# Kernel tuning notes

Measured on AMD Instinct MI355X. Metric: run time of the kernel, lower is better.

The kernel has to match this reference:

```python
import jax, jax.numpy as jnp
import numpy as np

BS, NUM_VISIT, MAX_FEAT, MAX_TARGET = 32, 6, 12, 16
NUM_FEAT, NUM_REL, HIDDEN, REDUCED, OUT = 1992, 11, 128, 256, 90
GAMMA = 0.1


def setup_inputs() -> dict:
    key = jax.random.key(0)
    ks = jax.random.split(key, 20)
    u = lambda k, shape: jax.random.uniform(k, shape, dtype=jnp.float32)
    # one/multi-hot-like dense float inputs (per docstring)
    feat_index = (u(ks[0], (BS, NUM_VISIT, MAX_FEAT, NUM_FEAT)) < 0.01).astype(jnp.float32)
    neighbor_index = (u(ks[1], (BS, NUM_VISIT, MAX_FEAT, MAX_TARGET, NUM_FEAT)) < 0.001).astype(jnp.float32)
    rel_index = (u(ks[2], (BS, NUM_VISIT, MAX_FEAT, MAX_TARGET, NUM_REL)) < 0.2).astype(jnp.float32)
    # parameters (torch.rand init in the original; xavier for embedding)
    bound = float(np.sqrt(6.0 / (NUM_FEAT + HIDDEN)))
    emb_weight = jax.random.uniform(ks[3], (NUM_FEAT, HIDDEN), dtype=jnp.float32, minval=-bound, maxval=bound)
    return {
        "feat_index": feat_index,
        "neighbor_index": neighbor_index,
        "rel_index": rel_index,
        "emb_weight": emb_weight,
        "W_edge": u(ks[4], (NUM_REL, HIDDEN)),
        "W_v": u(ks[5], (REDUCED, HIDDEN)),
        "W_r": u(ks[6], (REDUCED, HIDDEN)),
        "b_v": u(ks[7], (REDUCED,)),
        "b_r": u(ks[8], (REDUCED,)),
        "W_alpha": u(ks[9], (NUM_FEAT,)),
        "b_alpha": u(ks[10], (MAX_FEAT,)),
        "W_beta": u(ks[11], (MAX_FEAT,)),
        "b_beta": u(ks[12], (NUM_VISIT,)),
        "W_l": u(ks[13], (REDUCED, REDUCED)),
        "b_l": u(ks[14], (REDUCED,)),
        "fc_W": u(ks[15], (OUT, 2 * REDUCED)) * 0.05,
        "fc_b": u(ks[16], (OUT,)) * 0.05,
    }


def reference(feat_index, neighbor_index, rel_index, emb_weight, W_edge, W_v, W_r,
              b_v, b_r, W_alpha, b_alpha, W_beta, b_beta, W_l, b_l, fc_W, fc_b):
    num_visit = feat_index.shape[1]
    # decay buffer lamb[i] = exp(-gamma*(num_visit - i))
    lamb = jnp.exp(-GAMMA * (num_visit - jnp.arange(num_visit, dtype=feat_index.dtype)))

    # node-level attention alpha: (b,v,m)
    alpha = jax.nn.softmax(jnp.einsum('n,bvmn->bvm', W_alpha, feat_index) + b_alpha)
    # visit-level attention beta: (b,v), modulated by temporal decay
    beta = jnp.tanh(jnp.einsum('m,bvm->bv', W_beta, alpha) + b_beta) * lamb

    # reduced node embeddings: (num_feat, reduced)
    reduced_emb = emb_weight @ W_v.T + b_v
    # attention-weighted neighbor aggregation; sum over targets t fused in
    attn = alpha * beta[:, :, None]                       # (b,v,m)
    node_agg = jnp.einsum('bvm,bvmtn,nr->bvmr', attn, neighbor_index, reduced_emb)

    # reduced edge (relation) embeddings: (num_rel, reduced)
    reduced_edge = W_edge @ W_r.T + b_r
    edge_agg = jnp.einsum('bvmtr,rd->bvmd', rel_index, reduced_edge)  # sum over t fused

    agg = node_agg + edge_agg                             # (b,v,m,reduced)
    # einsum('dd, bvfd -> bvfd') in torch takes the diagonal of W_l
    h = jax.nn.relu(jnp.diagonal(W_l) * agg + b_l)        # (b,v,m,reduced)

    h_g = h.sum(axis=(1, 2))                              # (b, reduced)
    # einsum('bvmn,bvmr->bvnr').sum(n).sum(v) == contract over v,m,n
    h_p = jnp.einsum('bvm,bvmr->br', feat_index.sum(-1), h)

    z_joint = jnp.concatenate([h_g, h_p], axis=-1)        # (b, 2*reduced)
    return jax.nn.sigmoid(z_joint @ fc_W.T + fc_b)
```

## Files before the change

kernel.cpp:

```cpp
#include <hip/hip_runtime.h>
#include <math.h>

#define BS   32
#define NV   6
#define MF   12
#define MT   16
#define NF   1992
#define NR   11
#define HID  128
#define RED  256
#define OUTD 90
#define GAMMA 0.1f
#define NZCAP 1024

typedef float f4_t __attribute__((ext_vector_type(4)));

#define WS_HG    0
#define WS_HP    (WS_HG + BS*RED)
#define WS_ATTN  (WS_HP + BS*RED)
#define WS_FSUM  (WS_ATTN + BS*NV*MF)
#define WS_REMB  (WS_FSUM + BS*NV*MF)
#define WS_REDGE (WS_REMB + NF*RED)
#define WS_WTV   (WS_REDGE + NR*RED)
#define WS_WTR   (WS_WTV + HID*RED)
#define WS_FCWT  (WS_WTR + HID*RED)
#define WS_DIAG  (WS_FCWT + 2*RED*OUTD)
#define WS_CNT   (WS_DIAG + RED)
#define WS_RSUM  (WS_CNT + BS*NV*MF)
#define WS_NZN   (WS_RSUM + BS*NV*MF*NR)
#define WS_NZV   (WS_NZN + BS*NV*MF*NZCAP)

#define STREAM_BLOCKS (BS*NV*MF)
#define N_ZERO (2*BS*RED)
#define N_WTV  (HID*RED)
#define N_WTR  (HID*RED)
#define N_FCWT (2*RED*OUTD)
#define N_DIAG RED
#define PREP_ELEMS (N_ZERO + N_WTV + N_WTR + N_FCWT + N_DIAG)
#define PREP_BLOCKS (PREP_ELEMS / 256)

__global__ __launch_bounds__(256) void k_stream_prep_attn(
        const float* __restrict__ nbr, const float* __restrict__ rel,
        const float* __restrict__ W_v, const float* __restrict__ W_r,
        const float* __restrict__ fc_W, const float* __restrict__ W_l,
        const float* __restrict__ feat, const float* __restrict__ W_alpha,
        const float* __restrict__ b_alpha, const float* __restrict__ W_beta,
        const float* __restrict__ b_beta,
        float* __restrict__ ws_base,
        float* __restrict__ WT_v, float* __restrict__ WT_r, float* __restrict__ fcWT,
        float* __restrict__ diag,
        int* __restrict__ cnt_g, float* __restrict__ rsum_g,
        int* __restrict__ nzn_g, float* __restrict__ nzv_g,
        float* __restrict__ attn_ws, float* __restrict__ fsum_ws) {
    int blk = blockIdx.x;
    int tid = threadIdx.x;

    if (blk < STREAM_BLOCKS) {
        int bvm = blk;
        __shared__ int   nz_n[NZCAP];
        __shared__ float nz_v[NZCAP];
        __shared__ int   cnt;
        if (tid == 0) cnt = 0;
        const f4_t* base = (const f4_t*)(nbr + (size_t)bvm * MT * NF);
        f4_t a0 = (f4_t)(0.f);
        f4_t a1 = (f4_t)(0.f);
        const bool has1 = (tid + 256) < (NF / 4);
        #pragma unroll 4
        for (int t = 0; t < MT; ++t) {
            const f4_t* r4 = base + t * (NF / 4);
            a0 += __builtin_nontemporal_load(r4 + tid);
            if (has1) a1 += __builtin_nontemporal_load(r4 + tid + 256);
        }
        float rs = 0.f;
        if (tid < NR) {
            const float* rb = rel + (size_t)bvm * MT * NR;
            #pragma unroll
            for (int t = 0; t < MT; ++t) rs += rb[t * NR + tid];
        }
        __syncthreads();
        int nb = tid * 4;
        #pragma unroll
        for (int c = 0; c < 4; ++c)
            if (a0[c] != 0.f) {
                int p = atomicAdd(&cnt, 1);
                if (p < NZCAP) { nz_n[p] = nb + c; nz_v[p] = a0[c]; }
            }
        if (has1) {
            nb = (tid + 256) * 4;
            #pragma unroll
            for (int c = 0; c < 4; ++c)
                if (a1[c] != 0.f) {
                    int p = atomicAdd(&cnt, 1);
                    if (p < NZCAP) { nz_n[p] = nb + c; nz_v[p] = a1[c]; }
                }
        }
        __syncthreads();
        int c = min(cnt, NZCAP);
        if (tid == 0) cnt_g[bvm] = c;
        if (tid < NR) rsum_g[bvm * NR + tid] = rs;
        for (int i = tid; i < c; i += 256) {
            nzn_g[bvm * NZCAP + i] = nz_n[i];
            nzv_g[bvm * NZCAP + i] = nz_v[i];
        }
        return;
    }
    blk -= STREAM_BLOCKS;

    if (blk < PREP_BLOCKS) {
        int i = blk * 256 + tid;
        if (i < N_ZERO) {
            ws_base[i] = 0.f;
        } else if (i < N_ZERO + N_WTV) {
            int j = i - N_ZERO;
            int k = j >> 8, r = j & 255;
            WT_v[j] = W_v[r * HID + k];
        } else if (i < N_ZERO + N_WTV + N_WTR) {
            int j = i - (N_ZERO + N_WTV);
            int k = j >> 8, r = j & 255;
            WT_r[j] = W_r[r * HID + k];
        } else if (i < N_ZERO + N_WTV + N_WTR + N_FCWT) {
            int j = i - (N_ZERO + N_WTV + N_WTR);
            int jj = j / OUTD, o = j - jj * OUTD;
            fcWT[j] = fc_W[o * (2 * RED) + jj];
        } else {
            int j = i - (N_ZERO + N_WTV + N_WTR + N_FCWT);
            diag[j] = W_l[(size_t)j * RED + j];
        }
        return;
    }

    int bv   = blk - PREP_BLOCKS;
    int v    = bv % NV;
    int wave = tid >> 6;
    int lane = tid & 63;
    __shared__ float dot12[MF], fs12[MF];
    const float* base = feat + (size_t)bv * MF * NF;
    for (int m = wave; m < MF; m += 4) {
        const float4* rw = (const float4*)(base + (size_t)m * NF);
        const float4* wa = (const float4*)W_alpha;
        float da = 0.f, fs = 0.f;
        for (int i = lane; i < NF / 4; i += 64) {
            float4 x = rw[i];
            float4 w = wa[i];
            da += w.x * x.x + w.y * x.y + w.z * x.z + w.w * x.w;
            fs += x.x + x.y + x.z + x.w;
        }
        #pragma unroll
        for (int off = 32; off > 0; off >>= 1) {
            da += __shfl_xor(da, off);
            fs += __shfl_xor(fs, off);
        }
        if (lane == 0) { dot12[m] = da; fs12[m] = fs; }
    }
    __syncthreads();
    if (tid == 0) {
        float logits[MF];
        float mx = -1e30f;
        for (int m = 0; m < MF; ++m) { logits[m] = dot12[m] + b_alpha[m]; mx = fmaxf(mx, logits[m]); }
        float s = 0.f;
        for (int m = 0; m < MF; ++m) { logits[m] = expf(logits[m] - mx); s += logits[m]; }
        float inv = 1.f / s;
        float bdot = 0.f;
        for (int m = 0; m < MF; ++m) { logits[m] *= inv; bdot += W_beta[m] * logits[m]; }
        float lamb = expf(-GAMMA * (float)(NV - v));
        float beta = tanhf(bdot + b_beta[v]) * lamb;
        for (int m = 0; m < MF; ++m) {
            attn_ws[bv * MF + m] = logits[m] * beta;
            fsum_ws[bv * MF + m] = fs12[m];
        }
    }
}

#define NPB 8
#define NODE_BLOCKS (NF / NPB)
__global__ __launch_bounds__(256) void k_reduce(
        const float* __restrict__ emb, const float* __restrict__ W_edge,
        const float* __restrict__ WT_v, const float* __restrict__ WT_r,
        const float* __restrict__ b_v, const float* __restrict__ b_r,
        float* __restrict__ remb, float* __restrict__ redge) {
    int blk = blockIdx.x;
    int tid = threadIdx.x;
    if (blk < NODE_BLOCKS) {
        __shared__ float rows[NPB][HID];
        int n0 = blk * NPB;
        for (int i = tid; i < NPB * HID; i += 256)
            rows[i >> 7][i & 127] = emb[(size_t)n0 * HID + i];
        __syncthreads();
        float bv0 = b_v[tid];
        float a0 = bv0, a1 = bv0, a2 = bv0, a3 = bv0;
        float a4 = bv0, a5 = bv0, a6 = bv0, a7 = bv0;
        #pragma unroll 4
        for (int k = 0; k < HID; ++k) {
            float w = WT_v[k * RED + tid];
            a0 += rows[0][k] * w;
            a1 += rows[1][k] * w;
            a2 += rows[2][k] * w;
            a3 += rows[3][k] * w;
            a4 += rows[4][k] * w;
            a5 += rows[5][k] * w;
            a6 += rows[6][k] * w;
            a7 += rows[7][k] * w;
        }
        float* dst = remb + (size_t)n0 * RED + tid;
        dst[0*RED] = a0; dst[1*RED] = a1; dst[2*RED] = a2; dst[3*RED] = a3;
        dst[4*RED] = a4; dst[5*RED] = a5; dst[6*RED] = a6; dst[7*RED] = a7;
    } else {
        int e = blk - NODE_BLOCKS;
        __shared__ float row[HID];
        if (tid < HID) row[tid] = W_edge[e * HID + tid];
        __syncthreads();
        float acc = b_r[tid];
        #pragma unroll 4
        for (int k = 0; k < HID; ++k)
            acc += row[k] * WT_r[k * RED + tid];
        redge[e * RED + tid] = acc;
    }
}

__global__ __launch_bounds__(256) void k_gather(
        const float* __restrict__ remb, const float* __restrict__ redge,
        const int* __restrict__ cnt_g, const float* __restrict__ rsum_g,
        const int* __restrict__ nzn_g, const float* __restrict__ nzv_g,
        const float* __restrict__ attn_ws, const float* __restrict__ fsum_ws,
        const float* __restrict__ diag, const float* __restrict__ b_l,
        float* __restrict__ h_g, float* __restrict__ h_p) {
    int bvm = blockIdx.x;
    int b   = bvm / (NV * MF);
    int tid = threadIdx.x;
    __shared__ int   nz_n[NZCAP];
    __shared__ float nz_v[NZCAP];
    __shared__ float rsum[NR];
    int c = cnt_g[bvm];
    if (tid < NR) rsum[tid] = rsum_g[bvm * NR + tid];
    for (int i = tid; i < c; i += 256) {
        nz_n[i] = nzn_g[bvm * NZCAP + i];
        nz_v[i] = nzv_g[bvm * NZCAP + i];
    }
    __syncthreads();
    int r = tid;
    float node = 0.f;
    for (int i = 0; i < c; ++i)
        node += nz_v[i] * remb[(size_t)nz_n[i] * RED + r];
    float edge = 0.f;
    #pragma unroll
    for (int j = 0; j < NR; ++j)
        edge += rsum[j] * redge[j * RED + r];
    float a  = attn_ws[bvm];
    float fs = fsum_ws[bvm];
    float agg = a * node + edge;
    float h = fmaxf(0.f, diag[r] * agg + b_l[r]);
    atomicAdd(&h_g[b * RED + r], h);
    atomicAdd(&h_p[b * RED + r], fs * h);
}

__global__ __launch_bounds__(256) void k_out(
        const float* __restrict__ h_g, const float* __restrict__ h_p,
        const float* __restrict__ fcWT, const float* __restrict__ fc_b,
        float* __restrict__ out) {
    int b   = blockIdx.x;
    int tid = threadIdx.x;
    __shared__ float z[2 * RED];
    __shared__ float part[2][OUTD];
    for (int j = tid; j < RED; j += 256) {
        z[j]       = h_g[b * RED + j];
        z[RED + j] = h_p[b * RED + j];
    }
    __syncthreads();
    int o = tid & 127, half = tid >> 7;
    if (o < OUTD) {
        float acc = 0.f;
        int j0 = half * RED;
        #pragma unroll 8
        for (int j = j0; j < j0 + RED; ++j)
            acc += z[j] * fcWT[j * OUTD + o];
        part[half][o] = acc;
    }
    __syncthreads();
    if (tid < OUTD) {
        float acc = part[0][tid] + part[1][tid] + fc_b[tid];
        out[b * OUTD + tid] = 1.f / (1.f + expf(-acc));
    }
}

extern "C" void kernel_launch(void* const* d_in, const int* in_sizes, int n_in,
                              void* d_out, int out_size, void* d_ws, size_t ws_size,
                              hipStream_t stream) {
    const float* feat    = (const float*)d_in[0];
    const float* nbr     = (const float*)d_in[1];
    const float* rel     = (const float*)d_in[2];
    const float* emb     = (const float*)d_in[3];
    const float* W_edge  = (const float*)d_in[4];
    const float* W_v     = (const float*)d_in[5];
    const float* W_r     = (const float*)d_in[6];
    const float* b_v     = (const float*)d_in[7];
    const float* b_r     = (const float*)d_in[8];
    const float* W_alpha = (const float*)d_in[9];
    const float* b_alpha = (const float*)d_in[10];
    const float* W_beta  = (const float*)d_in[11];
    const float* b_beta  = (const float*)d_in[12];
    const float* W_l     = (const float*)d_in[13];
    const float* b_l     = (const float*)d_in[14];
    const float* fc_W    = (const float*)d_in[15];
    const float* fc_b    = (const float*)d_in[16];

    float* ws    = (float*)d_ws;
    float* hg    = ws + WS_HG;
    float* hp    = ws + WS_HP;
    float* attn  = ws + WS_ATTN;
    float* fsum  = ws + WS_FSUM;
    float* remb  = ws + WS_REMB;
    float* redge = ws + WS_REDGE;
    float* WT_v  = ws + WS_WTV;
    float* WT_r  = ws + WS_WTR;
    float* fcWT  = ws + WS_FCWT;
    float* diag  = ws + WS_DIAG;
    int*   cnt_g = (int*)(ws + WS_CNT);
    float* rsum_g= ws + WS_RSUM;
    int*   nzn_g = (int*)(ws + WS_NZN);
    float* nzv_g = ws + WS_NZV;

    k_stream_prep_attn<<<STREAM_BLOCKS + PREP_BLOCKS + BS * NV, 256, 0, stream>>>(
        nbr, rel, W_v, W_r, fc_W, W_l, feat, W_alpha, b_alpha, W_beta, b_beta,
        ws, WT_v, WT_r, fcWT, diag, cnt_g, rsum_g, nzn_g, nzv_g, attn, fsum);
    k_reduce<<<NODE_BLOCKS + NR, 256, 0, stream>>>(
        emb, W_edge, WT_v, WT_r, b_v, b_r, remb, redge);
    k_gather<<<BS * NV * MF, 256, 0, stream>>>(
        remb, redge, cnt_g, rsum_g, nzn_g, nzv_g, attn, fsum, diag, b_l, hg, hp);
    k_out<<<BS, 256, 0, stream>>>(hg, hp, fcWT, fc_b, (float*)d_out);
}
```

Baseline: 450.8 us.

## Fuse neighbor streaming into gather and merge prep with embedding reduction

The neighbor-index streaming and nonzero compaction move into the gather kernel, so the nonzero lists stay in shared memory instead of going through global memory. The embedding and relation reductions are folded into the first kernel and read transposed weights through shared-memory tiles, which removes the separate transpose pass. This cuts one launch and the global write/read of the nonzero lists. The nonzero cap is halved, which assumes the compacted list per row stays small, and the gather loop gets four independent accumulators.

```diff
diff --git a/kernel.cpp b/kernel.cpp
--- a/kernel.cpp
+++ b/kernel.cpp
@@ -11,7 +11,7 @@
 #define RED  256
 #define OUTD 90
 #define GAMMA 0.1f
-#define NZCAP 1024
+#define NZCAP 512
 
 typedef float f4_t __attribute__((ext_vector_type(4)));
 
@@ -21,206 +21,145 @@
 #define WS_FSUM  (WS_ATTN + BS*NV*MF)
 #define WS_REMB  (WS_FSUM + BS*NV*MF)
 #define WS_REDGE (WS_REMB + NF*RED)
-#define WS_WTV   (WS_REDGE + NR*RED)
-#define WS_WTR   (WS_WTV + HID*RED)
-#define WS_FCWT  (WS_WTR + HID*RED)
+#define WS_FCWT  (WS_REDGE + NR*RED)
 #define WS_DIAG  (WS_FCWT + 2*RED*OUTD)
-#define WS_CNT   (WS_DIAG + RED)
-#define WS_RSUM  (WS_CNT + BS*NV*MF)
-#define WS_NZN   (WS_RSUM + BS*NV*MF*NR)
-#define WS_NZV   (WS_NZN + BS*NV*MF*NZCAP)
-
-#define STREAM_BLOCKS (BS*NV*MF)
+
 #define N_ZERO (2*BS*RED)
-#define N_WTV  (HID*RED)
-#define N_WTR  (HID*RED)
 #define N_FCWT (2*RED*OUTD)
-#define N_DIAG RED
-#define PREP_ELEMS (N_ZERO + N_WTV + N_WTR + N_FCWT + N_DIAG)
-#define PREP_BLOCKS (PREP_ELEMS / 256)
-
-__global__ __launch_bounds__(256) void k_stream_prep_attn(
-        const float* __restrict__ nbr, const float* __restrict__ rel,
-        const float* __restrict__ W_v, const float* __restrict__ W_r,
-        const float* __restrict__ fc_W, const float* __restrict__ W_l,
+#define ZERO_BLOCKS (N_ZERO/256)
+#define PREP2_BLOCKS ((N_FCWT+RED)/256)
+#define ATTN_BLOCKS (BS*NV)
+#define NPB 8
+#define REMB_BLOCKS (NF/NPB)
+#define REDGE_BLOCKS 2
+#define K1_BLOCKS (ZERO_BLOCKS+PREP2_BLOCKS+ATTN_BLOCKS+REMB_BLOCKS+REDGE_BLOCKS)
+
+__global__ __launch_bounds__(256) void k1_prep_attn_reduce(
         const float* __restrict__ feat, const float* __restrict__ W_alpha,
         const float* __restrict__ b_alpha, const float* __restrict__ W_beta,
         const float* __restrict__ b_beta,
-        float* __restrict__ ws_base,
-        float* __restrict__ WT_v, float* __restrict__ WT_r, float* __restrict__ fcWT,
+        const float* __restrict__ emb, const float* __restrict__ W_edge,
+        const float* __restrict__ W_v, const float* __restrict__ W_r,
+        const float* __restrict__ b_v, const float* __restrict__ b_r,
+        const float* __restrict__ fc_W, const float* __restrict__ W_l,
+        float* __restrict__ ws_base, float* __restrict__ fcWT,
         float* __restrict__ diag,
-        int* __restrict__ cnt_g, float* __restrict__ rsum_g,
-        int* __restrict__ nzn_g, float* __restrict__ nzv_g,
-        float* __restrict__ attn_ws, float* __restrict__ fsum_ws) {
-    int blk = blockIdx.x;
-    int tid = threadIdx.x;
-
-    if (blk < STREAM_BLOCKS) {
-        int bvm = blk;
-        __shared__ int   nz_n[NZCAP];
-        __shared__ float nz_v[NZCAP];
-        __shared__ int   cnt;
-        if (tid == 0) cnt = 0;
-        const f4_t* base = (const f4_t*)(nbr + (size_t)bvm * MT * NF);
-        f4_t a0 = (f4_t)(0.f);
-        f4_t a1 = (f4_t)(0.f);
-        const bool has1 = (tid + 256) < (NF / 4);
-        #pragma unroll 4
-        for (int t = 0; t < MT; ++t) {
-            const f4_t* r4 = base + t * (NF / 4);
-            a0 += __builtin_nontemporal_load(r4 + tid);
-            if (has1) a1 += __builtin_nontemporal_load(r4 + tid + 256);
-        }
-        float rs = 0.f;
-        if (tid < NR) {
-            const float* rb = rel + (size_t)bvm * MT * NR;
-            #pragma unroll
-            for (int t = 0; t < MT; ++t) rs += rb[t * NR + tid];
-        }
-        __syncthreads();
-        int nb = tid * 4;
-        #pragma unroll
-        for (int c = 0; c < 4; ++c)
-            if (a0[c] != 0.f) {
-                int p = atomicAdd(&cnt, 1);
-                if (p < NZCAP) { nz_n[p] = nb + c; nz_v[p] = a0[c]; }
-            }
-        if (has1) {
-            nb = (tid + 256) * 4;
-            #pragma unroll
-            for (int c = 0; c < 4; ++c)
-                if (a1[c] != 0.f) {
-                    int p = atomicAdd(&cnt, 1);
-                    if (p < NZCAP) { nz_n[p] = nb + c; nz_v[p] = a1[c]; }
-                }
-        }
-        __syncthreads();
-        int c = min(cnt, NZCAP);
-        if (tid == 0) cnt_g[bvm] = c;
-        if (tid < NR) rsum_g[bvm * NR + tid] = rs;
-        for (int i = tid; i < c; i += 256) {
-            nzn_g[bvm * NZCAP + i] = nz_n[i];
-            nzv_g[bvm * NZCAP + i] = nz_v[i];
-        }
-        return;
-    }
-    blk -= STREAM_BLOCKS;
-
-    if (blk < PREP_BLOCKS) {
-        int i = blk * 256 + tid;
-        if (i < N_ZERO) {
-            ws_base[i] = 0.f;
-        } else if (i < N_ZERO + N_WTV) {
-            int j = i - N_ZERO;
-            int k = j >> 8, r = j & 255;
-            WT_v[j] = W_v[r * HID + k];
-        } else if (i < N_ZERO + N_WTV + N_WTR) {
-            int j = i - (N_ZERO + N_WTV);
-            int k = j >> 8, r = j & 255;
-            WT_r[j] = W_r[r * HID + k];
-        } else if (i < N_ZERO + N_WTV + N_WTR + N_FCWT) {
-            int j = i - (N_ZERO + N_WTV + N_WTR);
-            int jj = j / OUTD, o = j - jj * OUTD;
-            fcWT[j] = fc_W[o * (2 * RED) + jj];
-        } else {
-            int j = i - (N_ZERO + N_WTV + N_WTR + N_FCWT);
-            diag[j] = W_l[(size_t)j * RED + j];
-        }
-        return;
-    }
-
-    int bv   = blk - PREP_BLOCKS;
-    int v    = bv % NV;
-    int wave = tid >> 6;
-    int lane = tid & 63;
-    __shared__ float dot12[MF], fs12[MF];
-    const float* base = feat + (size_t)bv * MF * NF;
-    for (int m = wave; m < MF; m += 4) {
-        const float4* rw = (const float4*)(base + (size_t)m * NF);
-        const float4* wa = (const float4*)W_alpha;
-        float da = 0.f, fs = 0.f;
-        for (int i = lane; i < NF / 4; i += 64) {
-            float4 x = rw[i];
-            float4 w = wa[i];
-            da += w.x * x.x + w.y * x.y + w.z * x.z + w.w * x.w;
-            fs += x.x + x.y + x.z + x.w;
-        }
-        #pragma unroll
-        for (int off = 32; off > 0; off >>= 1) {
-            da += __shfl_xor(da, off);
-            fs += __shfl_xor(fs, off);
-        }
-        if (lane == 0) { dot12[m] = da; fs12[m] = fs; }
-    }
-    __syncthreads();
-    if (tid == 0) {
-        float logits[MF];
-        float mx = -1e30f;
-        for (int m = 0; m < MF; ++m) { logits[m] = dot12[m] + b_alpha[m]; mx = fmaxf(mx, logits[m]); }
-        float s = 0.f;
-        for (int m = 0; m < MF; ++m) { logits[m] = expf(logits[m] - mx); s += logits[m]; }
-        float inv = 1.f / s;
-        float bdot = 0.f;
-        for (int m = 0; m < MF; ++m) { logits[m] *= inv; bdot += W_beta[m] * logits[m]; }
-        float lamb = expf(-GAMMA * (float)(NV - v));
-        float beta = tanhf(bdot + b_beta[v]) * lamb;
-        for (int m = 0; m < MF; ++m) {
-            attn_ws[bv * MF + m] = logits[m] * beta;
-            fsum_ws[bv * MF + m] = fs12[m];
-        }
-    }
-}
-
-#define NPB 8
-#define NODE_BLOCKS (NF / NPB)
-__global__ __launch_bounds__(256) void k_reduce(
-        const float* __restrict__ emb, const float* __restrict__ W_edge,
-        const float* __restrict__ WT_v, const float* __restrict__ WT_r,
-        const float* __restrict__ b_v, const float* __restrict__ b_r,
+        float* __restrict__ attn_ws, float* __restrict__ fsum_ws,
         float* __restrict__ remb, float* __restrict__ redge) {
     int blk = blockIdx.x;
     int tid = threadIdx.x;
-    if (blk < NODE_BLOCKS) {
-        __shared__ float rows[NPB][HID];
-        int n0 = blk * NPB;
-        for (int i = tid; i < NPB * HID; i += 256)
-            rows[i >> 7][i & 127] = emb[(size_t)n0 * HID + i];
+
+    __shared__ float dot12[MF], fs12[MF];
+    __shared__ float rows[NPB][HID];
+    __shared__ float wT[32][RED + 1];
+
+    if (blk < ZERO_BLOCKS) {
+        ws_base[blk * 256 + tid] = 0.f;
+        return;
+    }
+    blk -= ZERO_BLOCKS;
+
+    if (blk < PREP2_BLOCKS) {
+        int i = blk * 256 + tid;
+        if (i < N_FCWT) {
+            int jj = i / OUTD, o = i - jj * OUTD;
+            fcWT[i] = fc_W[o * (2 * RED) + jj];
+        } else {
+            int j = i - N_FCWT;
+            diag[j] = W_l[(size_t)j * RED + j];
+        }
+        return;
+    }
+    blk -= PREP2_BLOCKS;
+
+    if (blk < ATTN_BLOCKS) {
+        int bv   = blk;
+        int v    = bv % NV;
+        int wave = tid >> 6;
+        int lane = tid & 63;
+        const float* base = feat + (size_t)bv * MF * NF;
+        for (int m = wave; m < MF; m += 4) {
+            const float4* rw = (const float4*)(base + (size_t)m * NF);
+            const float4* wa = (const float4*)W_alpha;
+            float da = 0.f, fs = 0.f;
+            for (int i = lane; i < NF / 4; i += 64) {
+                float4 x = rw[i];
+                float4 w = wa[i];
+                da += w.x * x.x + w.y * x.y + w.z * x.z + w.w * x.w;
+                fs += x.x + x.y + x.z + x.w;
+            }
+            #pragma unroll
+            for (int off = 32; off > 0; off >>= 1) {
+                da += __shfl_xor(da, off);
+                fs += __shfl_xor(fs, off);
+            }
+            if (lane == 0) { dot12[m] = da; fs12[m] = fs; }
+        }
         __syncthreads();
-        float bv0 = b_v[tid];
-        float a0 = bv0, a1 = bv0, a2 = bv0, a3 = bv0;
-        float a4 = bv0, a5 = bv0, a6 = bv0, a7 = bv0;
-        #pragma unroll 4
-        for (int k = 0; k < HID; ++k) {
-            float w = WT_v[k * RED + tid];
-            a0 += rows[0][k] * w;
-            a1 += rows[1][k] * w;
-            a2 += rows[2][k] * w;
-            a3 += rows[3][k] * w;
-            a4 += rows[4][k] * w;
-            a5 += rows[5][k] * w;
-            a6 += rows[6][k] * w;
-            a7 += rows[7][k] * w;
-        }
-        float* dst = remb + (size_t)n0 * RED + tid;
-        dst[0*RED] = a0; dst[1*RED] = a1; dst[2*RED] = a2; dst[3*RED] = a3;
-        dst[4*RED] = a4; dst[5*RED] = a5; dst[6*RED] = a6; dst[7*RED] = a7;
-    } else {
-        int e = blk - NODE_BLOCKS;
-        __shared__ float row[HID];
-        if (tid < HID) row[tid] = W_edge[e * HID + tid];
+        if (tid == 0) {
+            float logits[MF];
+            float mx = -1e30f;
+            for (int m = 0; m < MF; ++m) { logits[m] = dot12[m] + b_alpha[m]; mx = fmaxf(mx, logits[m]); }
+            float s = 0.f;
+            for (int m = 0; m < MF; ++m) { logits[m] = expf(logits[m] - mx); s += logits[m]; }
+            float inv = 1.f / s;
+            float bdot = 0.f;
+            for (int m = 0; m < MF; ++m) { logits[m] *= inv; bdot += W_beta[m] * logits[m]; }
+            float lamb = expf(-GAMMA * (float)(NV - v));
+            float beta = tanhf(bdot + b_beta[v]) * lamb;
+            for (int m = 0; m < MF; ++m) {
+                attn_ws[bv * MF + m] = logits[m] * beta;
+                fsum_ws[bv * MF + m] = fs12[m];
+            }
+        }
+        return;
+    }
+    blk -= ATTN_BLOCKS;
+
+    bool isEdge = (blk >= REMB_BLOCKS);
+    const float* src  = isEdge ? W_edge : emb;
+    const float* Wm   = isEdge ? W_r : W_v;
+    const float* bias = isEdge ? b_r : b_v;
+    float* dst        = isEdge ? redge : remb;
+    int n0    = (isEdge ? (blk - REMB_BLOCKS) : blk) * NPB;
+    int rowsN = isEdge ? min(NPB, NR - n0) : NPB;
+
+    for (int idx = tid; idx < rowsN * HID; idx += 256)
+        rows[idx >> 7][idx & 127] = src[(size_t)n0 * HID + idx];
+
+    float bb = bias[tid];
+    float a0 = bb, a1 = bb, a2 = bb, a3 = bb, a4 = bb, a5 = bb, a6 = bb, a7 = bb;
+    for (int k0 = 0; k0 < HID; k0 += 32) {
+        for (int idx = tid; idx < 32 * RED; idx += 256) {
+            int rr = idx >> 5, kk = idx & 31;
+            wT[kk][rr] = Wm[rr * HID + k0 + kk];
+        }
         __syncthreads();
-        float acc = b_r[tid];
-        #pragma unroll 4
-        for (int k = 0; k < HID; ++k)
-            acc += row[k] * WT_r[k * RED + tid];
-        redge[e * RED + tid] = acc;
-    }
+        #pragma unroll
+        for (int kk = 0; kk < 32; ++kk) {
+            float w = wT[kk][tid];
+            int k = k0 + kk;
+            a0 += rows[0][k] * w; a1 += rows[1][k] * w;
+            a2 += rows[2][k] * w; a3 += rows[3][k] * w;
+            a4 += rows[4][k] * w; a5 += rows[5][k] * w;
+            a6 += rows[6][k] * w; a7 += rows[7][k] * w;
+        }
+        __syncthreads();
+    }
+    float* d0 = dst + (size_t)n0 * RED + tid;
+    if (0 < rowsN) d0[0 * RED] = a0;
+    if (1 < rowsN) d0[1 * RED] = a1;
+    if (2 < rowsN) d0[2 * RED] = a2;
+    if (3 < rowsN) d0[3 * RED] = a3;
+    if (4 < rowsN) d0[4 * RED] = a4;
+    if (5 < rowsN) d0[5 * RED] = a5;
+    if (6 < rowsN) d0[6 * RED] = a6;
+    if (7 < rowsN) d0[7 * RED] = a7;
 }
 
-__global__ __launch_bounds__(256) void k_gather(
+__global__ __launch_bounds__(256) void k2_stream_gather(
+        const float* __restrict__ nbr, const float* __restrict__ rel,
         const float* __restrict__ remb, const float* __restrict__ redge,
-        const int* __restrict__ cnt_g, const float* __restrict__ rsum_g,
-        const int* __restrict__ nzn_g, const float* __restrict__ nzv_g,
         const float* __restrict__ attn_ws, const float* __restrict__ fsum_ws,
         const float* __restrict__ diag, const float* __restrict__ b_l,
         float* __restrict__ h_g, float* __restrict__ h_p) {
@@ -229,28 +168,75 @@
     int tid = threadIdx.x;
     __shared__ int   nz_n[NZCAP];
     __shared__ float nz_v[NZCAP];
-    __shared__ float rsum[NR];
-    int c = cnt_g[bvm];
-    if (tid < NR) rsum[tid] = rsum_g[bvm * NR + tid];
-    for (int i = tid; i < c; i += 256) {
-        nz_n[i] = nzn_g[bvm * NZCAP + i];
-        nz_v[i] = nzv_g[bvm * NZCAP + i];
+    __shared__ float rsum_s[NR];
+    __shared__ int   cnt;
+    __shared__ float s_attn, s_fsum;
+    if (tid == 0) { cnt = 0; s_attn = attn_ws[bvm]; s_fsum = fsum_ws[bvm]; }
+
+    int r = tid;
+    float dg = diag[r];
+    float bl = b_l[r];
+    float rg[NR];
+    #pragma unroll
+    for (int j = 0; j < NR; ++j) rg[j] = redge[j * RED + r];
+
+    const f4_t* base = (const f4_t*)(nbr + (size_t)bvm * MT * NF);
+    f4_t a0 = (f4_t)(0.f);
+    f4_t a1 = (f4_t)(0.f);
+    const bool has1 = (tid + 256) < (NF / 4);
+    #pragma unroll 4
+    for (int t = 0; t < MT; ++t) {
+        const f4_t* r4 = base + t * (NF / 4);
+        a0 += __builtin_nontemporal_load(r4 + tid);
+        if (has1) a1 += __builtin_nontemporal_load(r4 + tid + 256);
+    }
+    float rs = 0.f;
+    if (tid < NR) {
+        const float* rb = rel + (size_t)bvm * MT * NR;
+        #pragma unroll
+        for (int t = 0; t < MT; ++t) rs += rb[t * NR + tid];
     }
     __syncthreads();
-    int r = tid;
-    float node = 0.f;
-    for (int i = 0; i < c; ++i)
-        node += nz_v[i] * remb[(size_t)nz_n[i] * RED + r];
+
+    int nb = tid * 4;
+    #pragma unroll
+    for (int c4 = 0; c4 < 4; ++c4)
+        if (a0[c4] != 0.f) {
+            int p = atomicAdd(&cnt, 1);
+            if (p < NZCAP) { nz_n[p] = nb + c4; nz_v[p] = a0[c4]; }
+        }
+    if (has1) {
+        nb = (tid + 256) * 4;
+        #pragma unroll
+        for (int c4 = 0; c4 < 4; ++c4)
+            if (a1[c4] != 0.f) {
+                int p = atomicAdd(&cnt, 1);
+                if (p < NZCAP) { nz_n[p] = nb + c4; nz_v[p] = a1[c4]; }
+            }
+    }
+    if (tid < NR) rsum_s[tid] = rs;
+    __syncthreads();
+
+    int c = min(cnt, NZCAP);
+    float g0 = 0.f, g1 = 0.f, g2 = 0.f, g3 = 0.f;
+    int i = 0;
+    for (; i + 4 <= c; i += 4) {
+        g0 += nz_v[i]     * remb[(size_t)nz_n[i]     * RED + r];
+        g1 += nz_v[i + 1] * remb[(size_t)nz_n[i + 1] * RED + r];
+        g2 += nz_v[i + 2] * remb[(size_t)nz_n[i + 2] * RED + r];
+        g3 += nz_v[i + 3] * remb[(size_t)nz_n[i + 3] * RED + r];
+    }
+    for (; i < c; ++i)
+        g0 += nz_v[i] * remb[(size_t)nz_n[i] * RED + r];
+    float node = (g0 + g1) + (g2 + g3);
     float edge = 0.f;
     #pragma unroll
-    for (int j = 0; j < NR; ++j)
-        edge += rsum[j] * redge[j * RED + r];
-    float a  = attn_ws[bvm];
-    float fs = fsum_ws[bvm];
-    float agg = a * node + edge;
-    float h = fmaxf(0.f, diag[r] * agg + b_l[r]);
+    for (int j = 0; j < NR; ++j) edge += rsum_s[j] * rg[j];
+
+    float agg = s_attn * node + edge;
+    float h = fmaxf(0.f, dg * agg + bl);
     atomicAdd(&h_g[b * RED + r], h);
-    atomicAdd(&h_p[b * RED + r], fs * h);
+    atomicAdd(&h_p[b * RED + r], s_fsum * h);
 }
 
 __global__ __launch_bounds__(256) void k_out(
@@ -310,21 +296,14 @@
     float* fsum  = ws + WS_FSUM;
     float* remb  = ws + WS_REMB;
     float* redge = ws + WS_REDGE;
-    float* WT_v  = ws + WS_WTV;
-    float* WT_r  = ws + WS_WTR;
     float* fcWT  = ws + WS_FCWT;
     float* diag  = ws + WS_DIAG;
-    int*   cnt_g = (int*)(ws + WS_CNT);
-    float* rsum_g= ws + WS_RSUM;
-    int*   nzn_g = (int*)(ws + WS_NZN);
-    float* nzv_g = ws + WS_NZV;
-
-    k_stream_prep_attn<<<STREAM_BLOCKS + PREP_BLOCKS + BS * NV, 256, 0, stream>>>(
-        nbr, rel, W_v, W_r, fc_W, W_l, feat, W_alpha, b_alpha, W_beta, b_beta,
-        ws, WT_v, WT_r, fcWT, diag, cnt_g, rsum_g, nzn_g, nzv_g, attn, fsum);
-    k_reduce<<<NODE_BLOCKS + NR, 256, 0, stream>>>(
-        emb, W_edge, WT_v, WT_r, b_v, b_r, remb, redge);
-    k_gather<<<BS * NV * MF, 256, 0, stream>>>(
-        remb, redge, cnt_g, rsum_g, nzn_g, nzv_g, attn, fsum, diag, b_l, hg, hp);
+
+    k1_prep_attn_reduce<<<K1_BLOCKS, 256, 0, stream>>>(
+        feat, W_alpha, b_alpha, W_beta, b_beta,
+        emb, W_edge, W_v, W_r, b_v, b_r, fc_W, W_l,
+        ws, fcWT, diag, attn, fsum, remb, redge);
+    k2_stream_gather<<<BS * NV * MF, 256, 0, stream>>>(
+        nbr, rel, remb, redge, attn, fsum, diag, b_l, hg, hp);
     k_out<<<BS, 256, 0, stream>>>(hg, hp, fcWT, fc_b, (float*)d_out);
 }
```

Measured after the change: 440.5 us. 1.02x faster.
